# Kernel optimization log

Measured on AMD Instinct MI355X. Metric: run time of the kernel, lower is better.

Reference implementation:

```python
import jax, jax.numpy as jnp
import numpy as np

N_NODES = 200000
N_GRAPHS = 1024
BN_EPS = 1e-5


def setup_inputs() -> dict:
    key = jax.random.key(0)
    ks = jax.random.split(key, 24)
    s = 0.05
    inp = {
        "x": jax.random.normal(ks[0], (N_NODES, 78), jnp.float32),
        "edge_index": jax.random.randint(ks[1], (2, 3200000), 0, N_NODES, jnp.int32),
        "batch": jnp.sort(jax.random.randint(ks[2], (N_NODES,), 0, N_GRAPHS, jnp.int32)),
        "target": jax.random.randint(ks[3], (N_GRAPHS, 1000), 0, 26, jnp.int32),
        "g1_w1": jax.random.normal(ks[4], (78, 32), jnp.float32) * s,
        "g1_b1": jnp.zeros((32,), jnp.float32),
        "g1_w2": jax.random.normal(ks[5], (32, 32), jnp.float32) * s,
        "g1_b2": jnp.zeros((32,), jnp.float32),
        "gW1": jax.random.normal(ks[6], (4, 32, 32), jnp.float32) * s,
        "gb1": jnp.zeros((4, 32), jnp.float32),
        "gW2": jax.random.normal(ks[7], (4, 32, 32), jnp.float32) * s,
        "gb2": jnp.zeros((4, 32), jnp.float32),
        "bn_gamma": jnp.ones((5, 32), jnp.float32),
        "bn_beta": jnp.zeros((5, 32), jnp.float32),
        "fcxd_w": jax.random.normal(ks[8], (32, 128), jnp.float32) * s,
        "fcxd_b": jnp.zeros((128,), jnp.float32),
        "embed_xt": jax.random.normal(ks[9], (26, 128), jnp.float32) * s,
        "conv_w": jax.random.normal(ks[10], (32, 1000, 8), jnp.float32) * 0.01,
        "conv_b": jnp.zeros((32,), jnp.float32),
        "fcxt_w": jax.random.normal(ks[11], (3872, 128), jnp.float32) * 0.01,
        "fcxt_b": jnp.zeros((128,), jnp.float32),
        "fc1_w": jax.random.normal(ks[12], (256, 1024), jnp.float32) * s,
        "fc1_b": jnp.zeros((1024,), jnp.float32),
        "fc2_w": jax.random.normal(ks[13], (1024, 256), jnp.float32) * s,
        "fc2_b": jnp.zeros((256,), jnp.float32),
        "out_w": jax.random.normal(ks[14], (256, 1), jnp.float32) * s,
        "out_b": jnp.zeros((1,), jnp.float32),
    }
    return inp


def _gin_layer(h, edge_index, W1, b1, W2, b2, gamma, beta):
    # GINConv (eps=0): mlp(x + sum_{j in N(i)} x_j), then ReLU then BatchNorm
    agg = jax.ops.segment_sum(h[edge_index[0]], edge_index[1], num_segments=N_NODES)
    z = h + agg
    z = jnp.maximum(z @ W1 + b1, 0.0) @ W2 + b2
    z = jnp.maximum(z, 0.0)
    mu = z.mean(axis=0)
    var = z.var(axis=0)
    return (z - mu) * jax.lax.rsqrt(var + BN_EPS) * gamma + beta


def reference(x, edge_index, batch, target,
              g1_w1, g1_b1, g1_w2, g1_b2,
              gW1, gb1, gW2, gb2, bn_gamma, bn_beta,
              fcxd_w, fcxd_b, embed_xt, conv_w, conv_b,
              fcxt_w, fcxt_b, fc1_w, fc1_b, fc2_w, fc2_b, out_w, out_b):
    # --- molecule GIN branch (dropout = identity at inference) ---
    h = _gin_layer(x, edge_index, g1_w1, g1_b1, g1_w2, g1_b2, bn_gamma[0], bn_beta[0])
    for i in range(4):
        h = _gin_layer(h, edge_index, gW1[i], gb1[i], gW2[i], gb2[i],
                       bn_gamma[i + 1], bn_beta[i + 1])
    # global add pool over graphs
    pooled = jax.ops.segment_sum(h, batch, num_segments=N_GRAPHS)  # [B,32]
    xd = jnp.maximum(pooled @ fcxd_w + fcxd_b, 0.0)                # [B,128]

    # --- protein branch: embed -> Conv1d(in_ch=seq_len=1000, k=8) -> linear ---
    e = embed_xt[target]                                            # [B,1000,128]
    conv = jax.lax.conv_general_dilated(
        e, conv_w, window_strides=(1,), padding='VALID',
        dimension_numbers=('NCH', 'OIH', 'NCH'))                    # [B,32,121]
    conv = conv + conv_b[None, :, None]
    xt = conv.reshape(conv.shape[0], -1) @ fcxt_w + fcxt_b          # [B,128]

    # --- combined dense head ---
    xc = jnp.concatenate([xd, xt], axis=1)                          # [B,256]
    xc = jnp.maximum(xc @ fc1_w + fc1_b, 0.0)
    xc = xc @ fc2_w + fc2_b
    return xc @ out_w + out_b                                       # [B,1]
```

## Files before the change

### kernel.cpp

```cpp
#include <hip/hip_runtime.h>

#define HID 32
#define BN_EPS 1e-5f
#define NBMAX 512
#define BSHIFT 9
#define SCAT_CH 8192
#define FSTRIDE 10240
#define FCAP 10240

static __device__ __forceinline__ int lbound(const int* a, int n, int key) {
    int lo = 0, hi = n;
    while (lo < hi) { int m = (lo + hi) >> 1; if (a[m] < key) lo = m + 1; else hi = m; }
    return lo;
}

static __device__ __forceinline__ unsigned packbf2(float a, float b) {
    unsigned ua = __float_as_uint(a), ub = __float_as_uint(b);
    ua = (ua + 0x7fffu + ((ua >> 16) & 1u)) >> 16;
    ub = (ub + 0x7fffu + ((ub >> 16) & 1u)) & 0xffff0000u;
    return ua | ub;
}
static __device__ __forceinline__ float lo_bf(unsigned v) { return __uint_as_float(v << 16); }
static __device__ __forceinline__ float hi_bf(unsigned v) { return __uint_as_float(v & 0xffff0000u); }

static __device__ __forceinline__ void addu4(float* a, uint4 v) {
    a[0] += lo_bf(v.x); a[1] += hi_bf(v.x);
    a[2] += lo_bf(v.y); a[3] += hi_bf(v.y);
    a[4] += lo_bf(v.z); a[5] += hi_bf(v.z);
    a[6] += lo_bf(v.w); a[7] += hi_bf(v.w);
}

__global__ void __launch_bounds__(256) k_bscatter(const int* __restrict__ ei,
                                                  int* __restrict__ gcur,
                                                  int* __restrict__ pairs, int E, int NB) {
    __shared__ int h[NBMAX];
    __shared__ int lb[NBMAX];
    int t = threadIdx.x;
    int c0 = blockIdx.x * SCAT_CH;
    int end = min(c0 + SCAT_CH, E);
    for (int i = t; i < NBMAX; i += 256) h[i] = 0;
    __syncthreads();
    for (int i = c0 + t; i < end; i += 256)
        atomicAdd(&h[ei[E + i] >> BSHIFT], 1);
    __syncthreads();
    for (int b = t; b < NB; b += 256) {
        int c = h[b];
        lb[b] = c ? atomicAdd(&gcur[b], c) : 0;
        h[b] = 0;
    }
    __syncthreads();
    for (int i = c0 + t; i < end; i += 256) {
        int src = ei[i], d = ei[E + i];
        int bkt = d >> BSHIFT;
        int r = atomicAdd(&h[bkt], 1);
        pairs[bkt * FSTRIDE + lb[bkt] + r] = src | ((d & 511) << 18);
    }
}

__global__ void __launch_bounds__(512) k_bscan(const int* __restrict__ gcur,
                                               int* __restrict__ bbase,
                                               int* __restrict__ rowstart,
                                               int N, int E, int NB) {
    __shared__ int s[512];
    int t = threadIdx.x;
    int v = (t < NB) ? gcur[t] : 0;
    s[t] = v; __syncthreads();
    for (int off = 1; off < 512; off <<= 1) {
        int u = (t >= off) ? s[t - off] : 0; __syncthreads();
        s[t] += u; __syncthreads();
    }
    int excl = s[t] - v;
    if (t < NB) bbase[t] = excl;
    if (t == NB - 1) bbase[NB] = s[t];
    if (t == 0) rowstart[N] = E;
}

__global__ void __launch_bounds__(512) k_bfinal(const int* __restrict__ pairs,
                                                const int* __restrict__ bbase,
                                                const int* __restrict__ gcur,
                                                int* __restrict__ rowstart,
                                                int* __restrict__ csr, int N) {
    __shared__ int h[512];
    __shared__ int sc[512];
    __shared__ int loc[FCAP];
    int t = threadIdx.x;
    int b = blockIdx.x;
    int base = bbase[b];
    int cnt = gcur[b];
    const int* bp = pairs + (size_t)b * FSTRIDE;
    h[t] = 0;
    __syncthreads();
    for (int i = t; i < cnt; i += 512) atomicAdd(&h[bp[i] >> 18], 1);
    __syncthreads();
    int v = h[t];
    sc[t] = v; __syncthreads();
    for (int off = 1; off < 512; off <<= 1) {
        int u = (t >= off) ? sc[t - off] : 0; __syncthreads();
        sc[t] += u; __syncthreads();
    }
    int excl = sc[t] - v;
    int node = b * 512 + t;
    if (node < N) rowstart[node] = base + excl;
    h[t] = excl;
    __syncthreads();
    bool fit = (cnt <= FCAP);
    for (int i = t; i < cnt; i += 512) {
        int p = bp[i];
        int r = atomicAdd(&h[p >> 18], 1);
        int src = p & 0x3ffff;
        if (fit) loc[r] = src; else csr[base + r] = src;
    }
    __syncthreads();
    if (fit)
        for (int i = t; i < cnt; i += 512) csr[base + i] = loc[i];
}

__global__ void __launch_bounds__(256) k_A1(const float* __restrict__ x,
                                            const float* __restrict__ W,
                                            unsigned* __restrict__ Ub, int N) {
    __shared__ float xl[64 * 79];
    __shared__ float wl[78 * 33];
    int t = threadIdx.x;
    int n0 = blockIdx.x * 64;
    for (int idx = t; idx < 78 * 32; idx += 256)
        wl[(idx >> 5) * 33 + (idx & 31)] = W[idx];
    long base = (long)n0 * 78;
    for (int idx = t; idx < 64 * 78; idx += 256) {
        long g = base + idx;
        xl[(idx / 78) * 79 + (idx % 78)] = (g < (long)N * 78) ? x[g] : 0.f;
    }
    __syncthreads();
    int jp = t & 15, rg = t >> 4;
    for (int rep = 0; rep < 4; rep++) {
        int n = rg + 16 * rep;
        int node = n0 + n;
        if (node >= N) break;
        float a0 = 0.f, a1 = 0.f;
        #pragma unroll
        for (int k = 0; k < 78; k++) {
            float xv = xl[n * 79 + k];
            a0 += xv * wl[k * 33 + 2 * jp];
            a1 += xv * wl[k * 33 + 2 * jp + 1];
        }
        Ub[(size_t)node * 16 + jp] = packbf2(a0, a1);
    }
}

__global__ void __launch_bounds__(256) k_A(const float* __restrict__ X,
                                           const float* __restrict__ W,
                                           const float* __restrict__ slot,
                                           unsigned* __restrict__ Ub, int N) {
    __shared__ float zl[128 * 33];
    __shared__ float ws[32 * 33];
    __shared__ float cw[32];
    int t = threadIdx.x;
    int n0 = blockIdx.x * 128;
    for (int idx = t; idx < 1024; idx += 256) {
        int k = idx >> 5, j = idx & 31;
        ws[k * 33 + j] = slot[512 + k] * W[idx];
    }
    if (t < 32) {
        float acc = 0.f;
        for (int k = 0; k < 32; k++) acc += slot[544 + k] * W[k * 32 + t];
        cw[t] = acc;
    }
    for (int idx = t; idx < 128 * 32; idx += 256) {
        long g = (long)n0 * 32 + idx;
        zl[(idx >> 5) * 33 + (idx & 31)] = (g < (long)N * 32) ? X[g] : 0.f;
    }
    __syncthreads();
    int jp = t & 15, rg = t >> 4;
    for (int rep = 0; rep < 8; rep++) {
        int n = rg + 16 * rep;
        int node = n0 + n;
        if (node >= N) break;
        float a0 = cw[2 * jp], a1 = cw[2 * jp + 1];
        #pragma unroll
        for (int k = 0; k < 32; k++) {
            float zv = zl[n * 33 + k];
            a0 += zv * ws[k * 33 + 2 * jp];
            a1 += zv * ws[k * 33 + 2 * jp + 1];
        }
        Ub[(size_t)node * 16 + jp] = packbf2(a0, a1);
    }
}

__global__ void __launch_bounds__(256) k_BCS(const uint4* __restrict__ Ub4,
                                             const int* __restrict__ rowstart,
                                             const int* __restrict__ csr,
                                             const float* __restrict__ b1,
                                             const float* __restrict__ W2,
                                             const float* __restrict__ b2,
                                             float* __restrict__ X,
                                             float* __restrict__ slot, int N) {
    __shared__ float ws[32 * 33];
    __shared__ float tl[64 * 33];
    __shared__ float redS[8][33];
    __shared__ float redQ[8][33];
    int t = threadIdx.x;
    for (int idx = t; idx < 1024; idx += 256)
        ws[(idx >> 5) * 33 + (idx & 31)] = W2[idx];

    int g = t >> 2, l = t & 3;
    int node = blockIdx.x * 64 + g;
    bool act = (node < N);
    int s0 = 0, s1 = 0;
    if (act) { s0 = rowstart[node]; s1 = rowstart[node + 1]; }
    float a[8] = {0.f, 0.f, 0.f, 0.f, 0.f, 0.f, 0.f, 0.f};
    if (act) addu4(a, Ub4[(size_t)node * 4 + l]);
    int e = s0;
    for (; e + 1 < s1; e += 2) {
        int sa = csr[e], sb = csr[e + 1];
        uint4 va = Ub4[(size_t)sa * 4 + l];
        uint4 vb = Ub4[(size_t)sb * 4 + l];
        addu4(a, va);
        addu4(a, vb);
    }
    if (e < s1) addu4(a, Ub4[(size_t)csr[e] * 4 + l]);

    int f0 = 8 * l;
    #pragma unroll
    for (int i = 0; i < 8; i++)
        tl[g * 33 + f0 + i] = fmaxf(a[i] + b1[f0 + i], 0.f);
    __syncthreads();

    int j = t & 31, rg2 = t >> 5;
    float ps = 0.f, pq = 0.f;
    for (int rep = 0; rep < 8; rep++) {
        int n = rg2 + 8 * rep;
        int nod2 = blockIdx.x * 64 + n;
        float acc = b2[j];
        #pragma unroll
        for (int k = 0; k < 32; k++) acc += tl[n * 33 + k] * ws[k * 33 + j];
        float xv = fmaxf(acc, 0.f);
        if (nod2 < N) {
            X[(size_t)nod2 * 32 + j] = xv;
            ps += xv; pq += xv * xv;
        }
    }
    redS[rg2][j] = ps; redQ[rg2][j] = pq;
    __syncthreads();
    if (t < 32) {
        float s = 0.f, q = 0.f;
        #pragma unroll
        for (int r = 0; r < 8; r++) { s += redS[r][t]; q += redQ[r][t]; }
        int rep = blockIdx.x & 7;
        atomicAdd(&slot[rep * 64 + t], s);
        atomicAdd(&slot[rep * 64 + 32 + t], q);
    }
}

__global__ void k_fin(float* __restrict__ slot, const float* __restrict__ gamma,
                      const float* __restrict__ beta, int N) {
    int j = threadIdx.x;
    if (j < 32) {
        float s = 0.f, q = 0.f;
        for (int r = 0; r < 8; r++) { s += slot[r * 64 + j]; q += slot[r * 64 + 32 + j]; }
        float mu = s / (float)N;
        float var = q / (float)N - mu * mu;
        float a = gamma[j] * rsqrtf(var + BN_EPS);
        slot[512 + j] = a;
        slot[544 + j] = beta[j] - mu * a;
    }
}

__global__ void __launch_bounds__(128) k_pool(const float* __restrict__ X,
                                              const int* __restrict__ batch,
                                              const float* __restrict__ slot,
                                              const float* __restrict__ fw,
                                              const float* __restrict__ fb,
                                              float* __restrict__ xc, int N) {
    __shared__ float red[4][32];
    __shared__ float pv[32];
    int g = blockIdx.x, t = threadIdx.x;
    int lo = lbound(batch, N, g);
    int hi = lbound(batch, N, g + 1);
    int j = t & 31, rs = t >> 5;
    float ps = 0.f;
    for (int i = lo + rs; i < hi; i += 4) ps += X[(size_t)i * 32 + j];
    red[rs][j] = ps; __syncthreads();
    if (t < 32) {
        float s = red[0][t] + red[1][t] + red[2][t] + red[3][t];
        pv[t] = s * slot[512 + t] + (float)(hi - lo) * slot[544 + t];
    }
    __syncthreads();
    float acc = fb[t];
    for (int k = 0; k < 32; k++) acc += pv[k] * fw[k * 128 + t];
    xc[g * 256 + t] = fmaxf(acc, 0.f);
}

__global__ void __launch_bounds__(128) k_F2(const float* __restrict__ Emb,
                                            const float* __restrict__ fcxt,
                                            float* __restrict__ F) {
    __shared__ float er[128];
    int bid = blockIdx.x;
    int v = bid >> 5, o = bid & 31;
    int t = threadIdx.x;
    er[t] = Emb[v * 128 + t];
    __syncthreads();
    float acc[8] = {0.f, 0.f, 0.f, 0.f, 0.f, 0.f, 0.f, 0.f};
    for (int p = 0; p < 121; p++) {
        float fv = fcxt[(o * 121 + p) * 128 + t];
        #pragma unroll
        for (int k = 0; k < 8; k++) acc[k] += er[p + k] * fv;
    }
    #pragma unroll
    for (int k = 0; k < 8; k++)
        F[((size_t)v * 256 + o * 8 + k) * 128 + t] = acc[k];
}

__global__ void __launch_bounds__(128) k_cb(const float* __restrict__ fcxt,
                                            const float* __restrict__ fb,
                                            const float* __restrict__ cb,
                                            float* __restrict__ cbias) {
    int o = blockIdx.x, t = threadIdx.x;
    float acc = 0.f;
    for (int p = 0; p < 121; p++) acc += fcxt[(o * 121 + p) * 128 + t];
    float val = cb[o] * acc;
    if (o == 0) val += fb[t];
    atomicAdd(&cbias[t], val);
}

__global__ void __launch_bounds__(256) k_wT(const float* __restrict__ cw,
                                            float* __restrict__ wt) {
    int ok = blockIdx.x;
    int o = ok >> 3, kk = ok & 7;
    for (int c = threadIdx.x; c < 1000; c += 256)
        wt[ok * 1000 + c] = cw[(o * 1000 + c) * 8 + kk];
}

__global__ void __launch_bounds__(256) k_D2(const float* __restrict__ wt,
                                            const float* __restrict__ F,
                                            unsigned* __restrict__ Dmb) {
    __shared__ float Fl[32][128];
    __shared__ float Wl[32][64];
    int v = blockIdx.y;
    int c0 = blockIdx.x * 64;
    int t = threadIdx.x;
    int jg = t & 31, j0 = jg * 4;
    int cg = t >> 5;
    float4 acc[8];
    #pragma unroll
    for (int i = 0; i < 8; i++) acc[i] = make_float4(0.f, 0.f, 0.f, 0.f);
    for (int chunk = 0; chunk < 8; chunk++) {
        int k0 = chunk * 32;
        __syncthreads();
        for (int idx = t; idx < 4096; idx += 256) {
            int k = idx >> 7, j = idx & 127;
            Fl[k][j] = F[((size_t)v * 256 + k0 + k) * 128 + j];
        }
        for (int idx = t; idx < 2048; idx += 256) {
            int k = idx >> 6, c = idx & 63;
            Wl[k][c] = (c0 + c < 1000) ? wt[(k0 + k) * 1000 + c0 + c] : 0.f;
        }
        __syncthreads();
        for (int k = 0; k < 32; k++) {
            float4 fv = *(const float4*)&Fl[k][j0];
            #pragma unroll
            for (int ci = 0; ci < 8; ci++) {
                float wv = Wl[k][cg * 8 + ci];
                acc[ci].x += wv * fv.x;
                acc[ci].y += wv * fv.y;
                acc[ci].z += wv * fv.z;
                acc[ci].w += wv * fv.w;
            }
        }
    }
    #pragma unroll
    for (int ci = 0; ci < 8; ci++) {
        int c = c0 + cg * 8 + ci;
        if (c < 1000) {
            uint2 pk;
            pk.x = packbf2(acc[ci].x, acc[ci].y);
            pk.y = packbf2(acc[ci].z, acc[ci].w);
            *(uint2*)&Dmb[((size_t)c * 26 + v) * 64 + jg * 2] = pk;
        }
    }
}

__global__ void __launch_bounds__(256) k_xt3(const int* __restrict__ target,
                                             const uint4* __restrict__ Dm4,
                                             const float* __restrict__ cbias,
                                             float* __restrict__ xc) {
    __shared__ int tl[1000];
    __shared__ float red[16][132];
    int b = blockIdx.x, t = threadIdx.x;
    for (int i = t; i < 1000; i += 256) tl[i] = target[(size_t)b * 1000 + i];
    __syncthreads();
    int cl = t >> 4;
    int jg = t & 15;
    float acc[8] = {0.f, 0.f, 0.f, 0.f, 0.f, 0.f, 0.f, 0.f};
    for (int c = cl; c < 1000; c += 16) {
        int v = tl[c];
        uint4 d = Dm4[((size_t)c * 26 + v) * 16 + jg];
        acc[0] += lo_bf(d.x); acc[1] += hi_bf(d.x);
        acc[2] += lo_bf(d.y); acc[3] += hi_bf(d.y);
        acc[4] += lo_bf(d.z); acc[5] += hi_bf(d.z);
        acc[6] += lo_bf(d.w); acc[7] += hi_bf(d.w);
    }
    #pragma unroll
    for (int fi = 0; fi < 8; fi++) red[cl][jg * 8 + fi] = acc[fi];
    __syncthreads();
    if (t < 128) {
        float s = 0.f;
        #pragma unroll
        for (int r = 0; r < 16; r++) s += red[r][t];
        xc[(size_t)b * 256 + 128 + t] = cbias[t] + s;
    }
}

__global__ void __launch_bounds__(256) k_fc1(const float* __restrict__ xc,
                                             const float* __restrict__ w,
                                             const float* __restrict__ bias,
                                             float* __restrict__ y1) {
    __shared__ float xl[16 * 256];
    int t = threadIdx.x;
    int q0 = blockIdx.x * 256, b0 = blockIdx.y * 16;
    for (int idx = t; idx < 4096; idx += 256) xl[idx] = xc[b0 * 256 + idx];
    __syncthreads();
    int ql = t & 63, q = q0 + ql * 4;
    int bg = t >> 6;
    float4 bv = *(const float4*)&bias[q];
    float4 acc0 = bv, acc1 = bv, acc2 = bv, acc3 = bv;
    const float* xr = &xl[bg * 4 * 256];
    #pragma unroll 4
    for (int k = 0; k < 256; k++) {
        float4 wv = *(const float4*)&w[k * 1024 + q];
        float x0 = xr[k], x1 = xr[256 + k], x2 = xr[512 + k], x3 = xr[768 + k];
        acc0.x += x0 * wv.x; acc0.y += x0 * wv.y; acc0.z += x0 * wv.z; acc0.w += x0 * wv.w;
        acc1.x += x1 * wv.x; acc1.y += x1 * wv.y; acc1.z += x1 * wv.z; acc1.w += x1 * wv.w;
        acc2.x += x2 * wv.x; acc2.y += x2 * wv.y; acc2.z += x2 * wv.z; acc2.w += x2 * wv.w;
        acc3.x += x3 * wv.x; acc3.y += x3 * wv.y; acc3.z += x3 * wv.z; acc3.w += x3 * wv.w;
    }
    int b = b0 + bg * 4;
    float4 r;
    r.x = fmaxf(acc0.x, 0.f); r.y = fmaxf(acc0.y, 0.f); r.z = fmaxf(acc0.z, 0.f); r.w = fmaxf(acc0.w, 0.f);
    *(float4*)&y1[(size_t)b * 1024 + q] = r;
    r.x = fmaxf(acc1.x, 0.f); r.y = fmaxf(acc1.y, 0.f); r.z = fmaxf(acc1.z, 0.f); r.w = fmaxf(acc1.w, 0.f);
    *(float4*)&y1[(size_t)(b + 1) * 1024 + q] = r;
    r.x = fmaxf(acc2.x, 0.f); r.y = fmaxf(acc2.y, 0.f); r.z = fmaxf(acc2.z, 0.f); r.w = fmaxf(acc2.w, 0.f);
    *(float4*)&y1[(size_t)(b + 2) * 1024 + q] = r;
    r.x = fmaxf(acc3.x, 0.f); r.y = fmaxf(acc3.y, 0.f); r.z = fmaxf(acc3.z, 0.f); r.w = fmaxf(acc3.w, 0.f);
    *(float4*)&y1[(size_t)(b + 3) * 1024 + q] = r;
}

__global__ void k_wcomb(const float* __restrict__ fc2w, const float* __restrict__ fc2b,
                        const float* __restrict__ ow, const float* __restrict__ ob,
                        float* __restrict__ wc) {
    int p = blockIdx.x * 256 + threadIdx.x;
    float acc = 0.f;
    for (int q = 0; q < 256; q++) acc += fc2w[p * 256 + q] * ow[q];
    wc[p] = acc;
    if (p == 0) {
        float bc = ob[0];
        for (int q = 0; q < 256; q++) bc += fc2b[q] * ow[q];
        wc[1024] = bc;
    }
}

__global__ void __launch_bounds__(256) k_out(const float* __restrict__ y1,
                                             const float* __restrict__ wc,
                                             float* __restrict__ out) {
    __shared__ float r[256];
    int b = blockIdx.x, t = threadIdx.x;
    float acc = 0.f;
    for (int p = t; p < 1024; p += 256) acc += y1[b * 1024 + p] * wc[p];
    r[t] = acc; __syncthreads();
    for (int off = 128; off > 0; off >>= 1) {
        if (t < off) r[t] += r[t + off];
        __syncthreads();
    }
    if (t == 0) out[b] = r[0] + wc[1024];
}

extern "C" void kernel_launch(void* const* d_in, const int* in_sizes, int n_in,
                              void* d_out, int out_size, void* d_ws, size_t ws_size,
                              hipStream_t stream) {
    const float* x     = (const float*)d_in[0];
    const int*   ei    = (const int*)d_in[1];
    const int*   batch = (const int*)d_in[2];
    const int*   targ  = (const int*)d_in[3];
    const float* g1w1  = (const float*)d_in[4];
    const float* g1b1  = (const float*)d_in[5];
    const float* g1w2  = (const float*)d_in[6];
    const float* g1b2  = (const float*)d_in[7];
    const float* gW1   = (const float*)d_in[8];
    const float* gb1   = (const float*)d_in[9];
    const float* gW2   = (const float*)d_in[10];
    const float* gb2   = (const float*)d_in[11];
    const float* gam   = (const float*)d_in[12];
    const float* bet   = (const float*)d_in[13];
    const float* fcxdw = (const float*)d_in[14];
    const float* fcxdb = (const float*)d_in[15];
    const float* emb   = (const float*)d_in[16];
    const float* convw = (const float*)d_in[17];
    const float* convb = (const float*)d_in[18];
    const float* fcxtw = (const float*)d_in[19];
    const float* fcxtb = (const float*)d_in[20];
    const float* fc1w  = (const float*)d_in[21];
    const float* fc1b  = (const float*)d_in[22];
    const float* fc2w  = (const float*)d_in[23];
    const float* fc2b  = (const float*)d_in[24];
    const float* outw  = (const float*)d_in[25];
    const float* outb  = (const float*)d_in[26];

    int N = in_sizes[2];
    int E = in_sizes[1] / 2;
    int B = in_sizes[3] / 1000;
    int NB = (N + 511) >> BSHIFT;

    char* ws = (char*)d_ws;
    size_t off = 0;
    auto alloc = [&](size_t bytes) -> void* {
        void* p = ws + off;
        off += (bytes + 255) & ~(size_t)255;
        return p;
    };
    int*   rowstart = (int*)alloc((size_t)(N + 1) * 4);
    int*   bbase    = (int*)alloc((NBMAX + 1) * 4);
    int*   gcur     = (int*)alloc(NBMAX * 4);
    int*   csr      = (int*)alloc((size_t)E * 4);
    float* X        = (float*)alloc((size_t)N * 32 * 4);
    int*   pairs    = (int*)X;
    unsigned* Ub    = (unsigned*)alloc((size_t)N * 16 * 4);
    float* stats    = (float*)alloc((size_t)5 * 640 * 4);
    float* xc       = (float*)alloc((size_t)B * 256 * 4);
    float* Fb       = (float*)alloc((size_t)26 * 256 * 128 * 4);
    unsigned* Dmb   = (unsigned*)alloc((size_t)1000 * 26 * 64 * 4);
    float* wt       = (float*)alloc((size_t)256 * 1000 * 4);
    float* cbias    = (float*)alloc(128 * 4);
    float* y1       = (float*)alloc((size_t)B * 1024 * 4);
    float* wc       = (float*)alloc(1025 * 4);

    hipMemsetAsync(gcur, 0, NBMAX * 4, stream);
    hipMemsetAsync(stats, 0, (size_t)5 * 640 * 4, stream);
    hipMemsetAsync(cbias, 0, 128 * 4, stream);

    k_bscatter<<<(E + SCAT_CH - 1) / SCAT_CH, 256, 0, stream>>>(ei, gcur, pairs, E, NB);
    k_bscan<<<1, 512, 0, stream>>>(gcur, bbase, rowstart, N, E, NB);
    k_bfinal<<<NB, 512, 0, stream>>>(pairs, bbase, gcur, rowstart, csr, N);

    k_A1<<<(N + 63) / 64, 256, 0, stream>>>(x, g1w1, Ub, N);
    k_BCS<<<(N + 63) / 64, 256, 0, stream>>>((const uint4*)Ub, rowstart, csr,
                                             g1b1, g1w2, g1b2, X, stats, N);
    k_fin<<<1, 32, 0, stream>>>(stats, gam, bet, N);

    for (int i = 0; i < 4; i++) {
        float* slotPrev = stats + (size_t)i * 640;
        float* slotCur  = stats + (size_t)(i + 1) * 640;
        k_A<<<(N + 127) / 128, 256, 0, stream>>>(X, gW1 + i * 1024, slotPrev, Ub, N);
        k_BCS<<<(N + 63) / 64, 256, 0, stream>>>((const uint4*)Ub, rowstart, csr,
                                                 gb1 + i * 32, gW2 + i * 1024,
                                                 gb2 + i * 32, X, slotCur, N);
        k_fin<<<1, 32, 0, stream>>>(slotCur, gam + (i + 1) * 32, bet + (i + 1) * 32, N);
    }

    k_pool<<<B, 128, 0, stream>>>(X, batch, stats + 4 * 640, fcxdw, fcxdb, xc, N);

    k_wT<<<256, 256, 0, stream>>>(convw, wt);
    k_F2<<<26 * 32, 128, 0, stream>>>(emb, fcxtw, Fb);
    k_cb<<<32, 128, 0, stream>>>(fcxtw, fcxtb, convb, cbias);
    dim3 gD(16, 26);
    k_D2<<<gD, 256, 0, stream>>>(wt, Fb, Dmb);
    k_xt3<<<B, 256, 0, stream>>>(targ, (const uint4*)Dmb, cbias, xc);

    dim3 g1(4, B / 16);
    k_fc1<<<g1, 256, 0, stream>>>(xc, fc1w, fc1b, y1);
    k_wcomb<<<4, 256, 0, stream>>>(fc2w, fc2b, outw, outb, wc);
    k_out<<<B, 256, 0, stream>>>(y1, wc, (float*)d_out);
}
```

Measured before the change: 799.6 us.

## Aggregate before first linear layer and fuse GIN layers into one kernel

For layers 2-5 the neighbour sum now runs over the previous layer's output, stored as fp16, before the first linear layer. BatchNorm folding and the degree-times-bias term are applied inside the fused BCS1 kernel, which removes the separate k_A and k_fin launches and the fp32 X round trip. Intermediates change from bf16 to fp16 storage, halving activation traffic, and the conv weight transpose kernel is folded into k_D2's loads. This trades extra per-block matmul work and fp16 range and precision risk for fewer launches and less memory traffic.

Result: no change. 804.0 us (+0.5%).

```diff
diff --git a/kernel.cpp b/kernel.cpp
--- a/kernel.cpp
+++ b/kernel.cpp
@@ -1,4 +1,5 @@
 #include <hip/hip_runtime.h>
+#include <hip/hip_fp16.h>
 
 #define HID 32
 #define BN_EPS 1e-5f
@@ -14,20 +15,27 @@
     return lo;
 }
 
-static __device__ __forceinline__ unsigned packbf2(float a, float b) {
-    unsigned ua = __float_as_uint(a), ub = __float_as_uint(b);
-    ua = (ua + 0x7fffu + ((ua >> 16) & 1u)) >> 16;
-    ub = (ub + 0x7fffu + ((ub >> 16) & 1u)) & 0xffff0000u;
-    return ua | ub;
-}
-static __device__ __forceinline__ float lo_bf(unsigned v) { return __uint_as_float(v << 16); }
-static __device__ __forceinline__ float hi_bf(unsigned v) { return __uint_as_float(v & 0xffff0000u); }
-
-static __device__ __forceinline__ void addu4(float* a, uint4 v) {
-    a[0] += lo_bf(v.x); a[1] += hi_bf(v.x);
-    a[2] += lo_bf(v.y); a[3] += hi_bf(v.y);
-    a[4] += lo_bf(v.z); a[5] += hi_bf(v.z);
-    a[6] += lo_bf(v.w); a[7] += hi_bf(v.w);
+static __device__ __forceinline__ unsigned packh2(float a, float b) {
+    __half2 h = __floats2half2_rn(a, b);
+    return *reinterpret_cast<unsigned*>(&h);
+}
+static __device__ __forceinline__ float lo_h(unsigned v) {
+    __half2 h = *reinterpret_cast<__half2*>(&v);
+    return __low2float(h);
+}
+static __device__ __forceinline__ float hi_h(unsigned v) {
+    __half2 h = *reinterpret_cast<__half2*>(&v);
+    return __high2float(h);
+}
+static __device__ __forceinline__ float h2f(unsigned short v) {
+    return __half2float(__ushort_as_half(v));
+}
+
+static __device__ __forceinline__ void addu4h(float* a, uint4 v) {
+    a[0] += lo_h(v.x); a[1] += hi_h(v.x);
+    a[2] += lo_h(v.y); a[3] += hi_h(v.y);
+    a[4] += lo_h(v.z); a[5] += hi_h(v.z);
+    a[6] += lo_h(v.w); a[7] += hi_h(v.w);
 }
 
 __global__ void __launch_bounds__(256) k_bscatter(const int* __restrict__ ei,
@@ -142,64 +150,26 @@
             a0 += xv * wl[k * 33 + 2 * jp];
             a1 += xv * wl[k * 33 + 2 * jp + 1];
         }
-        Ub[(size_t)node * 16 + jp] = packbf2(a0, a1);
-    }
-}
-
-__global__ void __launch_bounds__(256) k_A(const float* __restrict__ X,
-                                           const float* __restrict__ W,
-                                           const float* __restrict__ slot,
-                                           unsigned* __restrict__ Ub, int N) {
-    __shared__ float zl[128 * 33];
-    __shared__ float ws[32 * 33];
-    __shared__ float cw[32];
-    int t = threadIdx.x;
-    int n0 = blockIdx.x * 128;
-    for (int idx = t; idx < 1024; idx += 256) {
-        int k = idx >> 5, j = idx & 31;
-        ws[k * 33 + j] = slot[512 + k] * W[idx];
-    }
-    if (t < 32) {
-        float acc = 0.f;
-        for (int k = 0; k < 32; k++) acc += slot[544 + k] * W[k * 32 + t];
-        cw[t] = acc;
-    }
-    for (int idx = t; idx < 128 * 32; idx += 256) {
-        long g = (long)n0 * 32 + idx;
-        zl[(idx >> 5) * 33 + (idx & 31)] = (g < (long)N * 32) ? X[g] : 0.f;
-    }
-    __syncthreads();
-    int jp = t & 15, rg = t >> 4;
-    for (int rep = 0; rep < 8; rep++) {
-        int n = rg + 16 * rep;
-        int node = n0 + n;
-        if (node >= N) break;
-        float a0 = cw[2 * jp], a1 = cw[2 * jp + 1];
-        #pragma unroll
-        for (int k = 0; k < 32; k++) {
-            float zv = zl[n * 33 + k];
-            a0 += zv * ws[k * 33 + 2 * jp];
-            a1 += zv * ws[k * 33 + 2 * jp + 1];
-        }
-        Ub[(size_t)node * 16 + jp] = packbf2(a0, a1);
-    }
-}
-
-__global__ void __launch_bounds__(256) k_BCS(const uint4* __restrict__ Ub4,
-                                             const int* __restrict__ rowstart,
-                                             const int* __restrict__ csr,
-                                             const float* __restrict__ b1,
-                                             const float* __restrict__ W2,
-                                             const float* __restrict__ b2,
-                                             float* __restrict__ X,
-                                             float* __restrict__ slot, int N) {
-    __shared__ float ws[32 * 33];
+        Ub[(size_t)node * 16 + jp] = packh2(a0, a1);
+    }
+}
+
+__global__ void __launch_bounds__(256) k_BCS0(const uint4* __restrict__ Ub4,
+                                              const int* __restrict__ rowstart,
+                                              const int* __restrict__ csr,
+                                              const float* __restrict__ b1,
+                                              const float* __restrict__ W2,
+                                              const float* __restrict__ b2,
+                                              unsigned* __restrict__ Outb,
+                                              float* __restrict__ slot, int N) {
+    __shared__ float w2s[32 * 33];
     __shared__ float tl[64 * 33];
+    __shared__ float ol[64 * 33];
     __shared__ float redS[8][33];
     __shared__ float redQ[8][33];
     int t = threadIdx.x;
     for (int idx = t; idx < 1024; idx += 256)
-        ws[(idx >> 5) * 33 + (idx & 31)] = W2[idx];
+        w2s[(idx >> 5) * 33 + (idx & 31)] = W2[idx];
 
     int g = t >> 2, l = t & 3;
     int node = blockIdx.x * 64 + g;
@@ -207,17 +177,16 @@
     int s0 = 0, s1 = 0;
     if (act) { s0 = rowstart[node]; s1 = rowstart[node + 1]; }
     float a[8] = {0.f, 0.f, 0.f, 0.f, 0.f, 0.f, 0.f, 0.f};
-    if (act) addu4(a, Ub4[(size_t)node * 4 + l]);
+    if (act) addu4h(a, Ub4[(size_t)node * 4 + l]);
     int e = s0;
     for (; e + 1 < s1; e += 2) {
         int sa = csr[e], sb = csr[e + 1];
         uint4 va = Ub4[(size_t)sa * 4 + l];
         uint4 vb = Ub4[(size_t)sb * 4 + l];
-        addu4(a, va);
-        addu4(a, vb);
-    }
-    if (e < s1) addu4(a, Ub4[(size_t)csr[e] * 4 + l]);
-
+        addu4h(a, va);
+        addu4h(a, vb);
+    }
+    if (e < s1) addu4h(a, Ub4[(size_t)csr[e] * 4 + l]);
     int f0 = 8 * l;
     #pragma unroll
     for (int i = 0; i < 8; i++)
@@ -231,12 +200,10 @@
         int nod2 = blockIdx.x * 64 + n;
         float acc = b2[j];
         #pragma unroll
-        for (int k = 0; k < 32; k++) acc += tl[n * 33 + k] * ws[k * 33 + j];
+        for (int k = 0; k < 32; k++) acc += tl[n * 33 + k] * w2s[k * 33 + j];
         float xv = fmaxf(acc, 0.f);
-        if (nod2 < N) {
-            X[(size_t)nod2 * 32 + j] = xv;
-            ps += xv; pq += xv * xv;
-        }
+        ol[n * 33 + j] = xv;
+        if (nod2 < N) { ps += xv; pq += xv * xv; }
     }
     redS[rg2][j] = ps; redQ[rg2][j] = pq;
     __syncthreads();
@@ -248,40 +215,149 @@
         atomicAdd(&slot[rep * 64 + t], s);
         atomicAdd(&slot[rep * 64 + 32 + t], q);
     }
-}
-
-__global__ void k_fin(float* __restrict__ slot, const float* __restrict__ gamma,
-                      const float* __restrict__ beta, int N) {
-    int j = threadIdx.x;
-    if (j < 32) {
+    for (int idx = t; idx < 1024; idx += 256) {
+        int n = idx >> 4, jp = idx & 15;
+        int nod = blockIdx.x * 64 + n;
+        if (nod < N)
+            Outb[(size_t)nod * 16 + jp] = packh2(ol[n * 33 + 2 * jp], ol[n * 33 + 2 * jp + 1]);
+    }
+}
+
+__global__ void __launch_bounds__(256) k_BCS1(const uint4* __restrict__ Xb4,
+                                              const int* __restrict__ rowstart,
+                                              const int* __restrict__ csr,
+                                              const float* __restrict__ pslot,
+                                              const float* __restrict__ pgam,
+                                              const float* __restrict__ pbet,
+                                              const float* __restrict__ W1,
+                                              const float* __restrict__ b1,
+                                              const float* __restrict__ W2,
+                                              const float* __restrict__ b2,
+                                              unsigned* __restrict__ Outb,
+                                              float* __restrict__ slot, int N) {
+    __shared__ float w1s[32 * 33];
+    __shared__ float w2s[32 * 33];
+    __shared__ float zl[64 * 33];
+    __shared__ float tl[64 * 33];
+    __shared__ float aa[32], cc[32], cw[32];
+    __shared__ float dp1[64];
+    __shared__ float redS[8][33];
+    __shared__ float redQ[8][33];
+    int t = threadIdx.x;
+    if (t < 32) {
         float s = 0.f, q = 0.f;
-        for (int r = 0; r < 8; r++) { s += slot[r * 64 + j]; q += slot[r * 64 + 32 + j]; }
+        #pragma unroll
+        for (int r = 0; r < 8; r++) { s += pslot[r * 64 + t]; q += pslot[r * 64 + 32 + t]; }
         float mu = s / (float)N;
         float var = q / (float)N - mu * mu;
-        float a = gamma[j] * rsqrtf(var + BN_EPS);
-        slot[512 + j] = a;
-        slot[544 + j] = beta[j] - mu * a;
-    }
-}
-
-__global__ void __launch_bounds__(128) k_pool(const float* __restrict__ X,
+        float av = pgam[t] * rsqrtf(var + BN_EPS);
+        aa[t] = av;
+        cc[t] = pbet[t] - mu * av;
+    }
+    __syncthreads();
+    for (int idx = t; idx < 1024; idx += 256) {
+        int k = idx >> 5, j = idx & 31;
+        w1s[k * 33 + j] = aa[k] * W1[idx];
+        w2s[k * 33 + j] = W2[idx];
+    }
+    if (t < 32) {
+        float acc = 0.f;
+        for (int k = 0; k < 32; k++) acc += cc[k] * W1[k * 32 + t];
+        cw[t] = acc;
+    }
+
+    int g = t >> 2, l = t & 3;
+    int node = blockIdx.x * 64 + g;
+    bool act = (node < N);
+    int s0 = 0, s1 = 0;
+    if (act) { s0 = rowstart[node]; s1 = rowstart[node + 1]; }
+    float a[8] = {0.f, 0.f, 0.f, 0.f, 0.f, 0.f, 0.f, 0.f};
+    if (act) addu4h(a, Xb4[(size_t)node * 4 + l]);
+    int e = s0;
+    for (; e + 1 < s1; e += 2) {
+        int sa = csr[e], sb = csr[e + 1];
+        uint4 va = Xb4[(size_t)sa * 4 + l];
+        uint4 vb = Xb4[(size_t)sb * 4 + l];
+        addu4h(a, va);
+        addu4h(a, vb);
+    }
+    if (e < s1) addu4h(a, Xb4[(size_t)csr[e] * 4 + l]);
+    int f0 = 8 * l;
+    #pragma unroll
+    for (int i = 0; i < 8; i++) zl[g * 33 + f0 + i] = a[i];
+    if (l == 0) dp1[g] = (float)(s1 - s0 + 1);
+    __syncthreads();
+
+    int j = t & 31, rg2 = t >> 5;
+    for (int rep = 0; rep < 8; rep++) {
+        int n = rg2 + 8 * rep;
+        float acc = dp1[n] * cw[j] + b1[j];
+        #pragma unroll
+        for (int k = 0; k < 32; k++) acc += zl[n * 33 + k] * w1s[k * 33 + j];
+        tl[n * 33 + j] = fmaxf(acc, 0.f);
+    }
+    __syncthreads();
+
+    float ps = 0.f, pq = 0.f;
+    for (int rep = 0; rep < 8; rep++) {
+        int n = rg2 + 8 * rep;
+        int nod2 = blockIdx.x * 64 + n;
+        float acc = b2[j];
+        #pragma unroll
+        for (int k = 0; k < 32; k++) acc += tl[n * 33 + k] * w2s[k * 33 + j];
+        float xv = fmaxf(acc, 0.f);
+        zl[n * 33 + j] = xv;
+        if (nod2 < N) { ps += xv; pq += xv * xv; }
+    }
+    redS[rg2][j] = ps; redQ[rg2][j] = pq;
+    __syncthreads();
+    if (t < 32) {
+        float s = 0.f, q = 0.f;
+        #pragma unroll
+        for (int r = 0; r < 8; r++) { s += redS[r][t]; q += redQ[r][t]; }
+        int rep = blockIdx.x & 7;
+        atomicAdd(&slot[rep * 64 + t], s);
+        atomicAdd(&slot[rep * 64 + 32 + t], q);
+    }
+    for (int idx = t; idx < 1024; idx += 256) {
+        int n = idx >> 4, jp = idx & 15;
+        int nod = blockIdx.x * 64 + n;
+        if (nod < N)
+            Outb[(size_t)nod * 16 + jp] = packh2(zl[n * 33 + 2 * jp], zl[n * 33 + 2 * jp + 1]);
+    }
+}
+
+__global__ void __launch_bounds__(128) k_pool(const unsigned short* __restrict__ Xb,
                                               const int* __restrict__ batch,
-                                              const float* __restrict__ slot,
+                                              const float* __restrict__ pslot,
+                                              const float* __restrict__ pgam,
+                                              const float* __restrict__ pbet,
                                               const float* __restrict__ fw,
                                               const float* __restrict__ fb,
                                               float* __restrict__ xc, int N) {
     __shared__ float red[4][32];
     __shared__ float pv[32];
+    __shared__ float aa[32], cc[32];
     int g = blockIdx.x, t = threadIdx.x;
+    if (t < 32) {
+        float s = 0.f, q = 0.f;
+        #pragma unroll
+        for (int r = 0; r < 8; r++) { s += pslot[r * 64 + t]; q += pslot[r * 64 + 32 + t]; }
+        float mu = s / (float)N;
+        float var = q / (float)N - mu * mu;
+        float av = pgam[t] * rsqrtf(var + BN_EPS);
+        aa[t] = av;
+        cc[t] = pbet[t] - mu * av;
+    }
     int lo = lbound(batch, N, g);
     int hi = lbound(batch, N, g + 1);
     int j = t & 31, rs = t >> 5;
     float ps = 0.f;
-    for (int i = lo + rs; i < hi; i += 4) ps += X[(size_t)i * 32 + j];
+    for (int i = lo + rs; i < hi; i += 4) ps += h2f(Xb[(size_t)i * 32 + j]);
     red[rs][j] = ps; __syncthreads();
     if (t < 32) {
         float s = red[0][t] + red[1][t] + red[2][t] + red[3][t];
-        pv[t] = s * slot[512 + t] + (float)(hi - lo) * slot[544 + t];
+        pv[t] = s * aa[t] + (float)(hi - lo) * cc[t];
     }
     __syncthreads();
     float acc = fb[t];
@@ -321,15 +397,7 @@
     atomicAdd(&cbias[t], val);
 }
 
-__global__ void __launch_bounds__(256) k_wT(const float* __restrict__ cw,
-                                            float* __restrict__ wt) {
-    int ok = blockIdx.x;
-    int o = ok >> 3, kk = ok & 7;
-    for (int c = threadIdx.x; c < 1000; c += 256)
-        wt[ok * 1000 + c] = cw[(o * 1000 + c) * 8 + kk];
-}
-
-__global__ void __launch_bounds__(256) k_D2(const float* __restrict__ wt,
+__global__ void __launch_bounds__(256) k_D2(const float* __restrict__ cw,
                                             const float* __restrict__ F,
                                             unsigned* __restrict__ Dmb) {
     __shared__ float Fl[32][128];
@@ -351,7 +419,8 @@
         }
         for (int idx = t; idx < 2048; idx += 256) {
             int k = idx >> 6, c = idx & 63;
-            Wl[k][c] = (c0 + c < 1000) ? wt[(k0 + k) * 1000 + c0 + c] : 0.f;
+            int ok = k0 + k;
+            Wl[k][c] = (c0 + c < 1000) ? cw[((ok >> 3) * 1000 + c0 + c) * 8 + (ok & 7)] : 0.f;
         }
         __syncthreads();
         for (int k = 0; k < 32; k++) {
@@ -371,8 +440,8 @@
         int c = c0 + cg * 8 + ci;
         if (c < 1000) {
             uint2 pk;
-            pk.x = packbf2(acc[ci].x, acc[ci].y);
-            pk.y = packbf2(acc[ci].z, acc[ci].w);
+            pk.x = packh2(acc[ci].x, acc[ci].y);
+            pk.y = packh2(acc[ci].z, acc[ci].w);
             *(uint2*)&Dmb[((size_t)c * 26 + v) * 64 + jg * 2] = pk;
         }
     }
@@ -393,10 +462,10 @@
     for (int c = cl; c < 1000; c += 16) {
         int v = tl[c];
         uint4 d = Dm4[((size_t)c * 26 + v) * 16 + jg];
-        acc[0] += lo_bf(d.x); acc[1] += hi_bf(d.x);
-        acc[2] += lo_bf(d.y); acc[3] += hi_bf(d.y);
-        acc[4] += lo_bf(d.z); acc[5] += hi_bf(d.z);
-        acc[6] += lo_bf(d.w); acc[7] += hi_bf(d.w);
+        acc[0] += lo_h(d.x); acc[1] += hi_h(d.x);
+        acc[2] += lo_h(d.y); acc[3] += hi_h(d.y);
+        acc[4] += lo_h(d.z); acc[5] += hi_h(d.z);
+        acc[6] += lo_h(d.w); acc[7] += hi_h(d.w);
     }
     #pragma unroll
     for (int fi = 0; fi < 8; fi++) red[cl][jg * 8 + fi] = acc[fi];
@@ -520,14 +589,17 @@
     int*   bbase    = (int*)alloc((NBMAX + 1) * 4);
     int*   gcur     = (int*)alloc(NBMAX * 4);
     int*   csr      = (int*)alloc((size_t)E * 4);
-    float* X        = (float*)alloc((size_t)N * 32 * 4);
-    int*   pairs    = (int*)X;
+    size_t xb_bytes = (size_t)N * 64;
+    size_t pairs_bytes = (size_t)NB * FSTRIDE * 4;
+    char*  blk      = (char*)alloc(2 * xb_bytes > pairs_bytes ? 2 * xb_bytes : pairs_bytes);
+    unsigned* XbA   = (unsigned*)blk;
+    unsigned* XbB   = (unsigned*)(blk + xb_bytes);
+    int*   pairs    = (int*)blk;
     unsigned* Ub    = (unsigned*)alloc((size_t)N * 16 * 4);
     float* stats    = (float*)alloc((size_t)5 * 640 * 4);
     float* xc       = (float*)alloc((size_t)B * 256 * 4);
     float* Fb       = (float*)alloc((size_t)26 * 256 * 128 * 4);
     unsigned* Dmb   = (unsigned*)alloc((size_t)1000 * 26 * 64 * 4);
-    float* wt       = (float*)alloc((size_t)256 * 1000 * 4);
     float* cbias    = (float*)alloc(128 * 4);
     float* y1       = (float*)alloc((size_t)B * 1024 * 4);
     float* wc       = (float*)alloc(1025 * 4);
@@ -540,28 +612,31 @@
     k_bscan<<<1, 512, 0, stream>>>(gcur, bbase, rowstart, N, E, NB);
     k_bfinal<<<NB, 512, 0, stream>>>(pairs, bbase, gcur, rowstart, csr, N);
 
+    int gBCS = (N + 63) / 64;
+
     k_A1<<<(N + 63) / 64, 256, 0, stream>>>(x, g1w1, Ub, N);
-    k_BCS<<<(N + 63) / 64, 256, 0, stream>>>((const uint4*)Ub, rowstart, csr,
-                                             g1b1, g1w2, g1b2, X, stats, N);
-    k_fin<<<1, 32, 0, stream>>>(stats, gam, bet, N);
-
+    k_BCS0<<<gBCS, 256, 0, stream>>>((const uint4*)Ub, rowstart, csr,
+                                     g1b1, g1w2, g1b2, XbA, stats, N);
+
+    unsigned* bufs[2] = {XbA, XbB};
     for (int i = 0; i < 4; i++) {
-        float* slotPrev = stats + (size_t)i * 640;
-        float* slotCur  = stats + (size_t)(i + 1) * 640;
-        k_A<<<(N + 127) / 128, 256, 0, stream>>>(X, gW1 + i * 1024, slotPrev, Ub, N);
-        k_BCS<<<(N + 63) / 64, 256, 0, stream>>>((const uint4*)Ub, rowstart, csr,
-                                                 gb1 + i * 32, gW2 + i * 1024,
-                                                 gb2 + i * 32, X, slotCur, N);
-        k_fin<<<1, 32, 0, stream>>>(slotCur, gam + (i + 1) * 32, bet + (i + 1) * 32, N);
-    }
-
-    k_pool<<<B, 128, 0, stream>>>(X, batch, stats + 4 * 640, fcxdw, fcxdb, xc, N);
-
-    k_wT<<<256, 256, 0, stream>>>(convw, wt);
+        unsigned* src = bufs[i & 1];
+        unsigned* dst = bufs[(i + 1) & 1];
+        k_BCS1<<<gBCS, 256, 0, stream>>>((const uint4*)src, rowstart, csr,
+                                         stats + (size_t)i * 640, gam + i * 32, bet + i * 32,
+                                         gW1 + i * 1024, gb1 + i * 32,
+                                         gW2 + i * 1024, gb2 + i * 32,
+                                         dst, stats + (size_t)(i + 1) * 640, N);
+    }
+
+    k_pool<<<B, 128, 0, stream>>>((const unsigned short*)XbA, batch,
+                                  stats + (size_t)4 * 640, gam + 128, bet + 128,
+                                  fcxdw, fcxdb, xc, N);
+
     k_F2<<<26 * 32, 128, 0, stream>>>(emb, fcxtw, Fb);
     k_cb<<<32, 128, 0, stream>>>(fcxtw, fcxtb, convb, cbias);
     dim3 gD(16, 26);
-    k_D2<<<gD, 256, 0, stream>>>(wt, Fb, Dmb);
+    k_D2<<<gD, 256, 0, stream>>>(convw, Fb, Dmb);
     k_xt3<<<B, 256, 0, stream>>>(targ, (const uint4*)Dmb, cbias, xc);
 
     dim3 g1(4, B / 16);
```
